# Optimization experiments

Measured on AMD Instinct MI355X. Metric: run time of the kernel, lower is better.

## Reference

```python
import jax, jax.numpy as jnp
import numpy as np

EPS = 1e-5
K_UP = 5      # k_upsample
SCALE = 2

def _conv(x, w, pad):
    # NCHW conv, no bias
    return jax.lax.conv_general_dilated(
        x, w, window_strides=(1, 1), padding=((pad, pad), (pad, pad)),
        dimension_numbers=('NCHW', 'OIHW', 'NCHW'))

def _bn(x, gamma, beta):
    # train-mode BatchNorm2d forward: batch stats over (N,H,W), biased var
    m = x.mean(axis=(0, 2, 3), keepdims=True)
    v = x.var(axis=(0, 2, 3), keepdims=True)
    xn = (x - m) * jax.lax.rsqrt(v + EPS)
    return xn * gamma[None, :, None, None] + beta[None, :, None, None]

def _pixel_shuffle(x, r):
    b, c, h, w = x.shape
    co = c // (r * r)
    x = x.reshape(b, co, r, r, h, w)
    x = x.transpose(0, 1, 4, 2, 5, 3)  # b, co, h, r, w, r
    return x.reshape(b, co, h * r, w * r)

def setup_inputs() -> dict:
    key = jax.random.key(0)
    ks = jax.random.split(key, 3)
    b, c, h, w = 8, 128, 64, 64
    mid = 64
    return {
        'x': jax.random.normal(ks[0], (b, c, h, w), jnp.float32),
        'comp_w': jax.random.normal(ks[1], (mid, c, 1, 1), jnp.float32) * (1.0 / np.sqrt(c)),
        'comp_g': jnp.ones((mid,), jnp.float32),
        'comp_b': jnp.zeros((mid,), jnp.float32),
        'enc_w': jax.random.normal(ks[2], ((K_UP * SCALE) ** 2, mid, 3, 3), jnp.float32) * (1.0 / np.sqrt(mid * 9)),
        'enc_g': jnp.ones(((K_UP * SCALE) ** 2,), jnp.float32),
        'enc_b': jnp.zeros(((K_UP * SCALE) ** 2,), jnp.float32),
    }

def reference(x, comp_w, comp_g, comp_b, enc_w, enc_g, enc_b):
    b, c, h, w = x.shape
    hm, wm = h * SCALE, w * SCALE
    # --- kernel prediction branch ---
    t = jax.nn.silu(_bn(_conv(x, comp_w, 0), comp_g, comp_b))        # [b,64,h,w]
    t = _bn(_conv(t, enc_w, 1), enc_g, enc_b)                        # [b,100,h,w] (act=False)
    t = _pixel_shuffle(t, SCALE)                                     # [b,25,hm,wm]
    wgt = jax.nn.softmax(t, axis=1)                                  # [b,25,hm,wm]
    # --- feature reassembly branch ---
    x_up = jnp.repeat(jnp.repeat(x, SCALE, axis=2), SCALE, axis=3)   # nearest upsample
    pad = (K_UP // 2) * SCALE  # = 4, preserves hm x wm with dilation=SCALE
    xp = jnp.pad(x_up, ((0, 0), (0, 0), (pad, pad), (pad, pad)))
    # unfold: kernel K_UP, dilation SCALE -> [b, c, 25, hm, wm], taps in (kh, kw) order
    patches = jnp.stack(
        [xp[:, :, dy * SCALE:dy * SCALE + hm, dx * SCALE:dx * SCALE + wm]
         for dy in range(K_UP) for dx in range(K_UP)], axis=2)
    # content-aware weighted sum over the 25 taps
    return jnp.einsum('bkhw,bckhw->bchw', wgt, patches)
```

## Files before the change

kernel.cpp:

```cpp
#include <hip/hip_runtime.h>
#include <hip/hip_bf16.h>
#include <math.h>

#define C_   128
#define HW_  4096
#define OC_  100
#define NSTAT_ 32768.0f

typedef __bf16 bf16x8 __attribute__((ext_vector_type(8)));
typedef __bf16 bf16x4 __attribute__((ext_vector_type(4)));
typedef float  f32x4  __attribute__((ext_vector_type(4)));

__global__ __launch_bounds__(256, 4) void k_conv1(const float* __restrict__ x,
                                                  const float* __restrict__ w,
                                                  const float* __restrict__ wenc,
                                                  __bf16* __restrict__ t1c,
                                                  float* __restrict__ csum,
                                                  float* __restrict__ csq,
                                                  __bf16* __restrict__ wprep) {
    __shared__ __bf16 xt[64 * 128];
    __shared__ __bf16 wt[64 * 128];
    __shared__ float sS[64], sQ[64];

    int blk = blockIdx.x;
    int b = blk & 7;
    int chunk = blk >> 3;
    int px0 = chunk * 64;
    int tid = threadIdx.x;
    if (tid < 64) { sS[tid] = 0.f; sQ[tid] = 0.f; }

    if (blk < 63) {
#pragma unroll
        for (int u = 0; u < 4; ++u) {
            int idx = blk * 1024 + u * 256 + tid;
            int oc = idx / 576, k = idx - oc * 576;
            int tap = k >> 6, ic = k & 63;
            wprep[idx] = (oc < OC_) ? (__bf16)wenc[((size_t)oc * 64 + ic) * 9 + tap]
                                    : (__bf16)0.f;
        }
    }

#pragma unroll
    for (int it = 0; it < 8; ++it) {
        int j = it * 256 + tid;
        int oc = j >> 5, f = j & 31;
        float4 v = *(const float4*)(w + (size_t)oc * 128 + f * 4);
        int blki = (f >> 1) ^ (oc & 15);
        bf16x4 st;
        st[0] = (__bf16)v.x; st[1] = (__bf16)v.y; st[2] = (__bf16)v.z; st[3] = (__bf16)v.w;
        *(bf16x4*)&wt[oc * 128 + blki * 8 + (f & 1) * 4] = st;
    }
#pragma unroll
    for (int it = 0; it < 2; ++it) {
        int j = it * 256 + tid;
        int px4 = (j & 15) * 4, icq = j >> 4;
        const float* xp = x + ((size_t)b * C_ + icq * 4) * HW_ + px0 + px4;
        float4 v0 = *(const float4*)(xp);
        float4 v1 = *(const float4*)(xp + HW_);
        float4 v2 = *(const float4*)(xp + 2 * HW_);
        float4 v3 = *(const float4*)(xp + 3 * HW_);
        float r0[4] = {v0.x, v0.y, v0.z, v0.w};
        float r1[4] = {v1.x, v1.y, v1.z, v1.w};
        float r2_[4] = {v2.x, v2.y, v2.z, v2.w};
        float r3[4] = {v3.x, v3.y, v3.z, v3.w};
#pragma unroll
        for (int r2 = 0; r2 < 4; ++r2) {
            int px = px4 + r2;
            int blki = (icq >> 1) ^ (px & 15);
            bf16x4 st;
            st[0] = (__bf16)r0[r2]; st[1] = (__bf16)r1[r2];
            st[2] = (__bf16)r2_[r2]; st[3] = (__bf16)r3[r2];
            *(bf16x4*)&xt[px * 128 + blki * 8 + (icq & 1) * 4] = st;
        }
    }
    __syncthreads();

    int lane = tid & 63, wv = tid >> 6;
    int p = lane & 15, q = lane >> 4;

    f32x4 acc[4];
#pragma unroll
    for (int n = 0; n < 4; ++n) acc[n] = (f32x4){0.f, 0.f, 0.f, 0.f};

#pragma unroll
    for (int kk = 0; kk < 4; ++kk) {
        int blki = (kk * 4 + q) ^ p;
        bf16x8 a = *(const bf16x8*)&xt[(wv * 16 + p) * 128 + blki * 8];
#pragma unroll
        for (int n = 0; n < 4; ++n) {
            bf16x8 bb = *(const bf16x8*)&wt[(n * 16 + p) * 128 + blki * 8];
            acc[n] = __builtin_amdgcn_mfma_f32_16x16x32_bf16(a, bb, acc[n], 0, 0, 0);
        }
    }

    __bf16* t1b = t1c + ((size_t)b * HW_ + px0 + wv * 16) * 64;
#pragma unroll
    for (int n = 0; n < 4; ++n) {
        float s = 0.f, qq = 0.f;
#pragma unroll
        for (int rg = 0; rg < 4; ++rg) {
            float v = acc[n][rg];
            t1b[(size_t)(q * 4 + rg) * 64 + n * 16 + p] = (__bf16)v;
            s += v; qq += v * v;
        }
        s += __shfl_down(s, 32, 64);  s += __shfl_down(s, 16, 64);
        qq += __shfl_down(qq, 32, 64); qq += __shfl_down(qq, 16, 64);
        if (lane < 16) {
            atomicAdd(&sS[n * 16 + p], s);
            atomicAdd(&sQ[n * 16 + p], qq);
        }
    }
    __syncthreads();
    if (tid < 64) {
        atomicAdd(&csum[tid], sS[tid]);
        atomicAdd(&csq[tid], sQ[tid]);
    }
}

__global__ __launch_bounds__(256, 4) void k_conv3(const __bf16* __restrict__ t1c,
                                                  const __bf16* __restrict__ wprep,
                                                  const float* __restrict__ csum,
                                                  const float* __restrict__ csq,
                                                  const float* __restrict__ cg,
                                                  const float* __restrict__ cb,
                                                  float* __restrict__ t2c,
                                                  float* __restrict__ esum,
                                                  float* __restrict__ esq) {
    __shared__ __bf16 xt[10 * 10 * 72];
    __shared__ float lsc[64], lsh[64];
    __shared__ float esuml[112], esql[112];

    int blk = blockIdx.x;
    int b = blk & 7;
    int tile = blk >> 3;
    int ty0 = (tile >> 3) * 8, tx0 = (tile & 7) * 8;
    int tid = threadIdx.x;
    if (tid < 112) { esuml[tid] = 0.f; esql[tid] = 0.f; }
    if (tid >= 128 && tid < 192) {
        int c = tid - 128;
        float invN = 1.0f / NSTAT_;
        float m = csum[c] * invN;
        float v = csq[c] * invN - m * m;
        float rs = rsqrtf(v + 1e-5f);
        float sc = cg[c] * rs;
        lsc[c] = sc;
        lsh[c] = cb[c] - m * sc;
    }
    __syncthreads();

    const __bf16* tb = t1c + (size_t)b * HW_ * 64;
#pragma unroll
    for (int it = 0; it < 7; ++it) {
        int idx = it * 256 + tid;
        if (idx < 1600) {
            int pxi = idx >> 4, f4 = idx & 15;
            int yy = pxi / 10, xx = pxi - yy * 10;
            int gy = ty0 + yy - 1, gx = tx0 + xx - 1;
            float o0 = 0.f, o1 = 0.f, o2 = 0.f, o3 = 0.f;
            if (gy >= 0 && gy < 64 && gx >= 0 && gx < 64) {
                bf16x4 v = *(const bf16x4*)(tb + ((size_t)(gy << 6) + gx) * 64 + f4 * 4);
                float4 sc = *(const float4*)(lsc + f4 * 4);
                float4 sh = *(const float4*)(lsh + f4 * 4);
                float u;
                u = fmaf((float)v[0], sc.x, sh.x); o0 = u / (1.f + __expf(-u));
                u = fmaf((float)v[1], sc.y, sh.y); o1 = u / (1.f + __expf(-u));
                u = fmaf((float)v[2], sc.z, sh.z); o2 = u / (1.f + __expf(-u));
                u = fmaf((float)v[3], sc.w, sh.w); o3 = u / (1.f + __expf(-u));
            }
            bf16x4 st;
            st[0] = (__bf16)o0; st[1] = (__bf16)o1; st[2] = (__bf16)o2; st[3] = (__bf16)o3;
            *(bf16x4*)&xt[pxi * 72 + f4 * 4] = st;
        }
    }
    __syncthreads();

    int lane = tid & 63, wv = tid >> 6;
    int p = lane & 15, q = lane >> 4;
    int ya = 2 * wv + (p >> 3), xa = p & 7;

    f32x4 acc[7];
#pragma unroll
    for (int n = 0; n < 7; ++n) acc[n] = (f32x4){0.f, 0.f, 0.f, 0.f};

#pragma unroll
    for (int kk = 0; kk < 18; ++kk) {
        const int tap = kk >> 1, ich = (kk & 1) * 32;
        const int ky = tap / 3, kx = tap - ky * 3;
        bf16x8 a0 = *(const bf16x8*)&xt[((ya + ky) * 10 + xa + kx) * 72 + ich + q * 8];
#pragma unroll
        for (int n = 0; n < 7; ++n) {
            bf16x8 bb = *(const bf16x8*)(wprep + ((size_t)(n * 16 + p)) * 576 + kk * 32 + q * 8);
            acc[n] = __builtin_amdgcn_mfma_f32_16x16x32_bf16(a0, bb, acc[n], 0, 0, 0);
        }
    }

    float* t2b = t2c + (size_t)b * HW_ * 112;
#pragma unroll
    for (int n = 0; n < 7; ++n) {
        float s = 0.f, qq = 0.f;
#pragma unroll
        for (int rg = 0; rg < 4; ++rg) {
            int mp = q * 4 + rg;
            int y = ty0 + 2 * wv + (mp >> 3), xo = tx0 + (mp & 7);
            float v = acc[n][rg];
            t2b[((size_t)y * 64 + xo) * 112 + n * 16 + p] = v;
            s += v; qq += v * v;
        }
        s += __shfl_down(s, 32, 64);  s += __shfl_down(s, 16, 64);
        qq += __shfl_down(qq, 32, 64); qq += __shfl_down(qq, 16, 64);
        if (lane < 16) {
            atomicAdd(&esuml[n * 16 + lane], s);
            atomicAdd(&esql[n * 16 + lane], qq);
        }
    }
    __syncthreads();
    if (tid < 112) {
        atomicAdd(&esum[tid], esuml[tid]);
        atomicAdd(&esq[tid], esql[tid]);
    }
}

__global__ __launch_bounds__(256, 4) void k_carafe(const float* __restrict__ x,
                                                   const float* __restrict__ t2c,
                                                   const float* __restrict__ esum,
                                                   const float* __restrict__ esq,
                                                   const float* __restrict__ eg,
                                                   const float* __restrict__ eb,
                                                   float* __restrict__ out) {
    __shared__ float xt[160 * 20];
    __shared__ float esc[112], esh[112];

    int blk = blockIdx.x;
    int b = blk & 7;
    int tile = blk >> 3;
    int tx0 = (tile & 3) * 16, ty0 = (tile >> 2) * 4;
    int tid = threadIdx.x;
    if (tid < 112) {
        float invN = 1.0f / NSTAT_;
        float m = esum[tid] * invN;
        float v = esq[tid] * invN - m * m;
        float rs = rsqrtf(v + 1e-5f);
        float sc = (tid < OC_) ? eg[tid] * rs : 0.f;
        esc[tid] = sc;
        esh[tid] = (tid < OC_) ? eb[tid] - m * sc : 0.f;
    }
    __syncthreads();

    int s = tid & 3, px = tid >> 2;
    int pxx = px & 15, py = px >> 4;
    int iy = ty0 + py, jx = tx0 + pxx;

    float wgt[25];
    {
        const float* t2p = t2c + ((size_t)((b << 12) + (iy << 6) + jx)) * 112 + s;
        float mx = -1e30f;
#pragma unroll
        for (int k = 0; k < 25; ++k) {
            float l = fmaf(t2p[k * 4], esc[4 * k + s], esh[4 * k + s]);
            wgt[k] = l;
            mx = fmaxf(mx, l);
        }
        float sum = 0.f;
#pragma unroll
        for (int k = 0; k < 25; ++k) {
            float e = __expf(wgt[k] - mx);
            wgt[k] = e;
            sum += e;
        }
        float inv = 1.f / sum;
#pragma unroll
        for (int k = 0; k < 25; ++k) wgt[k] *= inv;
    }

    const float* xb = x + (size_t)b * C_ * HW_;
    int i0 = iy * 2 + (s >> 1), j0 = jx * 2 + (s & 1);
    float* op = out + (size_t)b * C_ * 16384 + (size_t)i0 * 128 + j0;

    for (int stage = 0; stage < 8; ++stage) {
        int cbase = stage * 16;
        __syncthreads();
#pragma unroll
        for (int it = 0; it < 3; ++it) {
            int idx = it * 256 + tid;
            if (idx < 640) {
                int c4 = idx / 160;
                int r2 = idx - c4 * 160;
                int yy = r2 / 20, xx = r2 - yy * 20;
                int gy = ty0 - 2 + yy, gx = tx0 - 2 + xx;
                f32x4 st = {0.f, 0.f, 0.f, 0.f};
                if (gy >= 0 && gy < 64 && gx >= 0 && gx < 64) {
                    size_t base = (size_t)(cbase + c4 * 4) * HW_ + (gy << 6) + gx;
                    st[0] = xb[base];
                    st[1] = xb[base + HW_];
                    st[2] = xb[base + 2 * HW_];
                    st[3] = xb[base + 3 * HW_];
                }
                *(f32x4*)&xt[r2 * 20 + c4 * 4] = st;
            }
        }
        __syncthreads();

        float acc[16];
#pragma unroll
        for (int e = 0; e < 16; ++e) acc[e] = 0.f;

#pragma unroll
        for (int dy = 0; dy < 5; ++dy)
#pragma unroll
            for (int dx = 0; dx < 5; ++dx) {
                int pxi = (py + dy) * 20 + pxx + dx;
                float wk = wgt[dy * 5 + dx];
#pragma unroll
                for (int c4 = 0; c4 < 4; ++c4) {
                    f32x4 xv = *(const f32x4*)&xt[pxi * 20 + c4 * 4];
                    acc[c4 * 4 + 0] = fmaf(wk, xv[0], acc[c4 * 4 + 0]);
                    acc[c4 * 4 + 1] = fmaf(wk, xv[1], acc[c4 * 4 + 1]);
                    acc[c4 * 4 + 2] = fmaf(wk, xv[2], acc[c4 * 4 + 2]);
                    acc[c4 * 4 + 3] = fmaf(wk, xv[3], acc[c4 * 4 + 3]);
                }
            }
#pragma unroll
        for (int e = 0; e < 16; ++e)
            op[(size_t)(cbase + e) * 16384] = acc[e];
    }
}

extern "C" void kernel_launch(void* const* d_in, const int* in_sizes, int n_in,
                              void* d_out, int out_size, void* d_ws, size_t ws_size,
                              hipStream_t stream) {
    const float* x      = (const float*)d_in[0];
    const float* comp_w = (const float*)d_in[1];
    const float* comp_g = (const float*)d_in[2];
    const float* comp_b = (const float*)d_in[3];
    const float* enc_w  = (const float*)d_in[4];
    const float* enc_g  = (const float*)d_in[5];
    const float* enc_b  = (const float*)d_in[6];
    float* out = (float*)d_out;

    float* ws = (float*)d_ws;
    __bf16* t1c = (__bf16*)ws;
    float* t2c  = ws + 1048576;
    float* st   = ws + 1048576 + 3670016;
    float* csum = st;
    float* csq  = st + 64;
    float* esum = st + 128;
    float* esq  = st + 240;
    __bf16* wprep = (__bf16*)(st + 352);

    hipMemsetAsync(st, 0, 352 * sizeof(float), stream);
    k_conv1<<<512, 256, 0, stream>>>(x, comp_w, enc_w, t1c, csum, csq, wprep);
    k_conv3<<<512, 256, 0, stream>>>(t1c, wprep, csum, csq, comp_g, comp_b, t2c, esum, esq);
    k_carafe<<<512, 256, 0, stream>>>(x, t2c, esum, esq, enc_g, enc_b, out);
}
```

Before: 178.5 us.

## Double-buffer conv3 weights and carafe tiles in LDS, split carafe channels across blocks

In k_conv3 the encoder weights are staged through a double-buffered LDS slice, with the next K-chunk prefetched into registers during the MFMAs, instead of each lane loading them straight from global memory. k_carafe now splits the 128 channels into two halves handled by separate blocks, which doubles the grid to 1024. It also double-buffers the x tile so the next stage's global loads overlap the current stage's FMA work. The costs are a __syncthreads per K step in conv3, more LDS and registers, and the softmax weights being recomputed in both channel-half blocks.

```diff
diff --git a/kernel.cpp b/kernel.cpp
--- a/kernel.cpp
+++ b/kernel.cpp
@@ -127,6 +127,7 @@
                                                   float* __restrict__ esum,
                                                   float* __restrict__ esq) {
     __shared__ __bf16 xt[10 * 10 * 72];
+    __shared__ __bf16 bt[2][112 * 32];
     __shared__ float lsc[64], lsh[64];
     __shared__ float esuml[112], esql[112];
 
@@ -147,6 +148,18 @@
         lsh[c] = cb[c] - m * sc;
     }
     __syncthreads();
+
+    {
+        int oc = tid >> 2, part = tid & 3;
+        *(bf16x8*)&bt[0][oc * 32 + part * 8] =
+            *(const bf16x8*)(wprep + (size_t)oc * 576 + part * 8);
+        if (tid < 192) {
+            int c1 = tid + 256;
+            int oc1 = c1 >> 2, p1 = c1 & 3;
+            *(bf16x8*)&bt[0][oc1 * 32 + p1 * 8] =
+                *(const bf16x8*)(wprep + (size_t)oc1 * 576 + p1 * 8);
+        }
+    }
 
     const __bf16* tb = t1c + (size_t)b * HW_ * 64;
 #pragma unroll
@@ -177,6 +190,8 @@
     int lane = tid & 63, wv = tid >> 6;
     int p = lane & 15, q = lane >> 4;
     int ya = 2 * wv + (p >> 3), xa = p & 7;
+    int soc = tid >> 2, spart = tid & 3;
+    int soc1 = (tid + 256) >> 2, spart1 = (tid + 256) & 3;
 
     f32x4 acc[7];
 #pragma unroll
@@ -184,13 +199,26 @@
 
 #pragma unroll
     for (int kk = 0; kk < 18; ++kk) {
+        const int cur = kk & 1;
+        bf16x8 r0, r1;
+        if (kk < 17) {
+            r0 = *(const bf16x8*)(wprep + (size_t)soc * 576 + (kk + 1) * 32 + spart * 8);
+            if (tid < 192)
+                r1 = *(const bf16x8*)(wprep + (size_t)soc1 * 576 + (kk + 1) * 32 + spart1 * 8);
+        }
         const int tap = kk >> 1, ich = (kk & 1) * 32;
         const int ky = tap / 3, kx = tap - ky * 3;
         bf16x8 a0 = *(const bf16x8*)&xt[((ya + ky) * 10 + xa + kx) * 72 + ich + q * 8];
 #pragma unroll
         for (int n = 0; n < 7; ++n) {
-            bf16x8 bb = *(const bf16x8*)(wprep + ((size_t)(n * 16 + p)) * 576 + kk * 32 + q * 8);
+            bf16x8 bb = *(const bf16x8*)&bt[cur][(n * 16 + p) * 32 + q * 8];
             acc[n] = __builtin_amdgcn_mfma_f32_16x16x32_bf16(a0, bb, acc[n], 0, 0, 0);
+        }
+        if (kk < 17) {
+            *(bf16x8*)&bt[1 - cur][soc * 32 + spart * 8] = r0;
+            if (tid < 192)
+                *(bf16x8*)&bt[1 - cur][soc1 * 32 + spart1 * 8] = r1;
+            __syncthreads();
         }
     }
 
@@ -227,12 +255,14 @@
                                                    const float* __restrict__ eg,
                                                    const float* __restrict__ eb,
                                                    float* __restrict__ out) {
-    __shared__ float xt[160 * 20];
+    __shared__ float xt[2][160 * 20];
     __shared__ float esc[112], esh[112];
 
     int blk = blockIdx.x;
     int b = blk & 7;
-    int tile = blk >> 3;
+    int r = blk >> 3;
+    int tile = r & 63;
+    int chalf = r >> 6;
     int tx0 = (tile & 3) * 16, ty0 = (tile >> 2) * 4;
     int tid = threadIdx.x;
     if (tid < 112) {
@@ -276,34 +306,63 @@
     int i0 = iy * 2 + (s >> 1), j0 = jx * 2 + (s & 1);
     float* op = out + (size_t)b * C_ * 16384 + (size_t)i0 * 128 + j0;
 
-    for (int stage = 0; stage < 8; ++stage) {
-        int cbase = stage * 16;
+    int sidx[3], sgy[3], sgx[3], sc4[3];
+#pragma unroll
+    for (int it = 0; it < 3; ++it) {
+        int idx = it * 256 + tid;
+        sidx[it] = idx;
+        int c4 = idx / 160;
+        int r2 = idx - c4 * 160;
+        int yy = r2 / 20, xx = r2 - yy * 20;
+        sgy[it] = ty0 - 2 + yy;
+        sgx[it] = tx0 - 2 + xx;
+        sc4[it] = c4;
+    }
+
+#pragma unroll
+    for (int it = 0; it < 3; ++it) {
+        if (sidx[it] < 640) {
+            int gy = sgy[it], gx = sgx[it];
+            f32x4 st = {0.f, 0.f, 0.f, 0.f};
+            if (gy >= 0 && gy < 64 && gx >= 0 && gx < 64) {
+                size_t base = (size_t)(chalf * 64 + sc4[it] * 4) * HW_ + (gy << 6) + gx;
+                st[0] = xb[base];
+                st[1] = xb[base + HW_];
+                st[2] = xb[base + 2 * HW_];
+                st[3] = xb[base + 3 * HW_];
+            }
+            int r2 = sidx[it] - sc4[it] * 160;
+            *(f32x4*)&xt[0][r2 * 20 + sc4[it] * 4] = st;
+        }
+    }
+
+#pragma unroll
+    for (int stage = 0; stage < 4; ++stage) {
+        int cur = stage & 1;
+        int cbase = chalf * 64 + stage * 16;
+        f32x4 pf[3];
+        if (stage < 3) {
+#pragma unroll
+            for (int it = 0; it < 3; ++it) {
+                if (sidx[it] < 640) {
+                    int gy = sgy[it], gx = sgx[it];
+                    f32x4 st = {0.f, 0.f, 0.f, 0.f};
+                    if (gy >= 0 && gy < 64 && gx >= 0 && gx < 64) {
+                        size_t base = (size_t)(cbase + 16 + sc4[it] * 4) * HW_ + (gy << 6) + gx;
+                        st[0] = xb[base];
+                        st[1] = xb[base + HW_];
+                        st[2] = xb[base + 2 * HW_];
+                        st[3] = xb[base + 3 * HW_];
+                    }
+                    pf[it] = st;
+                }
+            }
+        }
         __syncthreads();
-#pragma unroll
-        for (int it = 0; it < 3; ++it) {
-            int idx = it * 256 + tid;
-            if (idx < 640) {
-                int c4 = idx / 160;
-                int r2 = idx - c4 * 160;
-                int yy = r2 / 20, xx = r2 - yy * 20;
-                int gy = ty0 - 2 + yy, gx = tx0 - 2 + xx;
-                f32x4 st = {0.f, 0.f, 0.f, 0.f};
-                if (gy >= 0 && gy < 64 && gx >= 0 && gx < 64) {
-                    size_t base = (size_t)(cbase + c4 * 4) * HW_ + (gy << 6) + gx;
-                    st[0] = xb[base];
-                    st[1] = xb[base + HW_];
-                    st[2] = xb[base + 2 * HW_];
-                    st[3] = xb[base + 3 * HW_];
-                }
-                *(f32x4*)&xt[r2 * 20 + c4 * 4] = st;
-            }
-        }
-        __syncthreads();
 
         float acc[16];
 #pragma unroll
         for (int e = 0; e < 16; ++e) acc[e] = 0.f;
-
 #pragma unroll
         for (int dy = 0; dy < 5; ++dy)
 #pragma unroll
@@ -312,7 +371,7 @@
                 float wk = wgt[dy * 5 + dx];
 #pragma unroll
                 for (int c4 = 0; c4 < 4; ++c4) {
-                    f32x4 xv = *(const f32x4*)&xt[pxi * 20 + c4 * 4];
+                    f32x4 xv = *(const f32x4*)&xt[cur][pxi * 20 + c4 * 4];
                     acc[c4 * 4 + 0] = fmaf(wk, xv[0], acc[c4 * 4 + 0]);
                     acc[c4 * 4 + 1] = fmaf(wk, xv[1], acc[c4 * 4 + 1]);
                     acc[c4 * 4 + 2] = fmaf(wk, xv[2], acc[c4 * 4 + 2]);
@@ -322,6 +381,16 @@
 #pragma unroll
         for (int e = 0; e < 16; ++e)
             op[(size_t)(cbase + e) * 16384] = acc[e];
+
+        if (stage < 3) {
+#pragma unroll
+            for (int it = 0; it < 3; ++it) {
+                if (sidx[it] < 640) {
+                    int r2 = sidx[it] - sc4[it] * 160;
+                    *(f32x4*)&xt[1 - cur][r2 * 20 + sc4[it] * 4] = pf[it];
+                }
+            }
+        }
     }
 }
 
@@ -350,5 +419,5 @@
     hipMemsetAsync(st, 0, 352 * sizeof(float), stream);
     k_conv1<<<512, 256, 0, stream>>>(x, comp_w, enc_w, t1c, csum, csq, wprep);
     k_conv3<<<512, 256, 0, stream>>>(t1c, wprep, csum, csq, comp_g, comp_b, t2c, esum, esq);
-    k_carafe<<<512, 256, 0, stream>>>(x, t2c, esum, esq, enc_g, enc_b, out);
+    k_carafe<<<1024, 256, 0, stream>>>(x, t2c, esum, esq, enc_g, enc_b, out);
 }
```

After: 154.0 us. 13.7% less time.
